# Kernel tuning notes

Measured on AMD Instinct MI355X. Metric: run time of the kernel, lower is better.

The kernel has to match this reference:

```python
import jax, jax.numpy as jnp
import numpy as np

HIDDEN = 1024
NH = 16
NKV = 8
HD = 128
ROPE_BASE = 1e6
EPS = 1e-6


def _rms_norm(x, w):
    # x: [..., HD], norm in fp32 like the torch module
    xf = x.astype(jnp.float32)
    var = jnp.mean(xf * xf, axis=-1, keepdims=True)
    return w * (xf * jax.lax.rsqrt(var + EPS)).astype(x.dtype)


def _rotate_half(x):
    h = x.shape[-1] // 2
    return jnp.concatenate([-x[..., h:], x[..., :h]], axis=-1)


def _rope_cos_sin(position_ids, dtype):
    inv_freq = 1.0 / (ROPE_BASE ** (jnp.arange(0, HD, 2, dtype=jnp.float32) / HD))
    freqs = position_ids.astype(jnp.float32)[:, None] * inv_freq[None, :]  # [S, HD/2]
    emb = jnp.concatenate([freqs, freqs], axis=-1)  # [S, HD]
    return jnp.cos(emb).astype(dtype), jnp.sin(emb).astype(dtype)


def setup_inputs() -> dict:
    key = jax.random.key(0)
    ks = jax.random.split(key, 7)
    B, S = 2, 2048
    scale = lambda fan_in: 1.0 / np.sqrt(fan_in)
    return {
        "hidden_states": jax.random.normal(ks[0], (B, S, HIDDEN), jnp.float32),
        "position_ids": jnp.arange(S, dtype=jnp.int32),
        "Wq": jax.random.normal(ks[1], (HIDDEN, NH * HD), jnp.float32) * scale(HIDDEN),
        "Wk": jax.random.normal(ks[2], (HIDDEN, NKV * HD), jnp.float32) * scale(HIDDEN),
        "Wv": jax.random.normal(ks[3], (HIDDEN, NKV * HD), jnp.float32) * scale(HIDDEN),
        "Wo": jax.random.normal(ks[4], (NH * HD, HIDDEN), jnp.float32) * scale(NH * HD),
        "q_norm_w": jnp.ones((HD,), jnp.float32),
        "k_norm_w": jnp.ones((HD,), jnp.float32),
    }


def reference(hidden_states, position_ids, Wq, Wk, Wv, Wo, q_norm_w, k_norm_w):
    B, S, _ = hidden_states.shape
    G = NH // NKV  # GQA group size

    q = (hidden_states @ Wq).reshape(B, S, NH, HD)
    k = (hidden_states @ Wk).reshape(B, S, NKV, HD)
    v = (hidden_states @ Wv).reshape(B, S, NKV, HD)

    q = _rms_norm(q, q_norm_w).transpose(0, 2, 1, 3)  # [B, NH, S, HD]
    k = _rms_norm(k, k_norm_w).transpose(0, 2, 1, 3)  # [B, NKV, S, HD]
    v = v.transpose(0, 2, 1, 3)                        # [B, NKV, S, HD]

    cos, sin = _rope_cos_sin(position_ids, q.dtype)    # [S, HD] each
    q = q * cos + _rotate_half(q) * sin
    k = k * cos + _rotate_half(k) * sin

    # GQA: broadcast KV heads across groups instead of repeat_interleave copies
    qg = q.reshape(B, NKV, G, S, HD)
    scores = jnp.einsum('bkgsd,bknd->bkgsn', qg, k) / jnp.sqrt(jnp.float32(HD))
    causal = jnp.tril(jnp.ones((S, S), dtype=bool))
    scores = jnp.where(causal, scores, -jnp.inf)
    attn = jax.nn.softmax(scores, axis=-1)
    out = jnp.einsum('bkgsn,bknd->bkgsd', attn, v)  # [B, NKV, G, S, HD]
    out = out.reshape(B, NH, S, HD).transpose(0, 2, 1, 3).reshape(B, S, NH * HD)
    return out @ Wo
```

## Files before the change

### kernel.cpp

```cpp
#include <hip/hip_runtime.h>
#include <cstdint>
#include <cstddef>

#define HIDDEN 1024
#define NH 16
#define NKV 8
#define HD 128
#define SEQ 2048
#define BATCH 2
#define NTOK (BATCH*SEQ)

typedef __bf16 bf16x8 __attribute__((ext_vector_type(8)));
typedef float f32x4 __attribute__((ext_vector_type(4)));

__device__ __forceinline__ unsigned short f2bf(float f) {
  unsigned int u = __float_as_uint(f);
  u += 0x7FFFu + ((u >> 16) & 1u);
  return (unsigned short)(u >> 16);
}
__device__ __forceinline__ float bf2f(unsigned short h) {
  return __uint_as_float(((unsigned int)h) << 16);
}

#if __has_builtin(__builtin_amdgcn_exp2f)
#define EXP2(x) __builtin_amdgcn_exp2f(x)
#else
#define EXP2(x) exp2f(x)
#endif

__device__ __forceinline__ void glds16(const unsigned short* g, unsigned short* l) {
  __builtin_amdgcn_global_load_lds(
      (const __attribute__((address_space(1))) unsigned int*)g,
      (__attribute__((address_space(3))) unsigned int*)l, 16, 0, 0);
}

#define WAIT_VM8()   __builtin_amdgcn_s_waitcnt(0x0F78)
#define WAIT_VM6()   __builtin_amdgcn_s_waitcnt(0x0F76)
#define WAIT_VM4()   __builtin_amdgcn_s_waitcnt(0x0F74)
#define WAIT_VM0()   __builtin_amdgcn_s_waitcnt(0x0F70)
#define WAIT_LGKM0() __builtin_amdgcn_s_waitcnt(0xC07F)
#define BARRIER()    __builtin_amdgcn_s_barrier()

__device__ __forceinline__ float dpp_addx1(float x) {
  int v = __builtin_amdgcn_update_dpp(0, __float_as_int(x), 0xB1, 0xF, 0xF, true);
  return x + __int_as_float(v);
}

__global__ __launch_bounds__(256) void tcvt_all_kernel(
    const float* __restrict__ Wq, const float* __restrict__ Wk,
    const float* __restrict__ Wv, const float* __restrict__ Wo,
    const float* __restrict__ hs,
    unsigned short* __restrict__ wqkvt, unsigned short* __restrict__ wot,
    unsigned short* __restrict__ hsb) {
  const int i = blockIdx.x;
  const int tx = threadIdx.x, ty = threadIdx.y;
  if (i >= 6144) {
    const int t = ty*32 + tx;
    const size_t base = (size_t)(i - 6144) * 1024;
#pragma unroll
    for (int j = 0; j < 4; ++j) {
      const size_t idx = base + j*256 + t;
      float4 v = ((const float4*)hs)[idx];
      ushort4 o;
      o.x = f2bf(v.x); o.y = f2bf(v.y); o.z = f2bf(v.z); o.w = f2bf(v.w);
      ((ushort4*)hsb)[idx] = o;
    }
    return;
  }
  __shared__ float tl[32][33];
  const float* src; unsigned short* dst; int R, C, r0, c0;
  if (i < 2048)      { int l = i;        src = Wq; dst = wqkvt;                      R = 1024; C = 2048; r0 = (l & 31)*32; c0 = (l >> 5)*32; }
  else if (i < 3072) { int l = i - 2048; src = Wk; dst = wqkvt + (size_t)2048*1024;  R = 1024; C = 1024; r0 = (l & 31)*32; c0 = (l >> 5)*32; }
  else if (i < 4096) { int l = i - 3072; src = Wv; dst = wqkvt + (size_t)3072*1024;  R = 1024; C = 1024; r0 = (l & 31)*32; c0 = (l >> 5)*32; }
  else               { int l = i - 4096; src = Wo; dst = wot;                        R = 2048; C = 1024; r0 = (l & 63)*32; c0 = (l >> 6)*32; }
#pragma unroll
  for (int k = 0; k < 4; ++k)
    tl[ty + 8*k][tx] = src[(size_t)(r0 + ty + 8*k)*C + c0 + tx];
  __syncthreads();
#pragma unroll
  for (int k = 0; k < 4; ++k)
    dst[(size_t)(c0 + ty + 8*k)*R + r0 + tx] = f2bf(tl[tx][ty + 8*k]);
}

__global__ __launch_bounds__(256) void gemm_qkv_fused_kernel(
    const unsigned short* __restrict__ A,
    const unsigned short* __restrict__ Bt,
    const float* __restrict__ qw, const float* __restrict__ kw,
    const int* __restrict__ pos_ids,
    unsigned short* __restrict__ q_l,
    unsigned short* __restrict__ k_l,
    unsigned short* __restrict__ vt8) {
  constexpr int BM = 128, BK = 64, K = 1024, NIT = K/BK;
  __shared__ __align__(16) char smem[70144];
  unsigned short* As0 = (unsigned short*)smem;
  unsigned short* Bs0 = (unsigned short*)(smem + 32768);
  float* ftile = (float*)smem;
  float* rinv  = (float*)(smem + 69632);

  const int t = threadIdx.x, lane = t & 63, w = t >> 6;
  const int l15 = lane & 15, l4 = lane >> 4;
  const int wr = (w >> 1)*64, wc = (w & 1)*64;
  const int m0 = blockIdx.x * BM, n0 = blockIdx.y * 128;
  const unsigned short* Ab = A + (size_t)m0*K;
  const unsigned short* Bb = Bt + (size_t)n0*K;

  const f32x4 vzero = {0.f, 0.f, 0.f, 0.f};
  f32x4 acc[4][4];
#pragma unroll
  for (int i = 0; i < 4; ++i)
#pragma unroll
    for (int j = 0; j < 4; ++j) acc[i][j] = vzero;

#pragma unroll
  for (int i = 0; i < 4; ++i) {
    const int c = (w*4 + i)*64 + lane;
    glds16(Ab + (size_t)(c >> 3)*K + (c & 7)*8, As0 + (size_t)(w*4 + i)*512);
  }
#pragma unroll
  for (int i = 0; i < 4; ++i) {
    const int c = (w*4 + i)*64 + lane;
    glds16(Bb + (size_t)(c >> 3)*K + (c & 7)*8, Bs0 + (size_t)(w*4 + i)*512);
  }

  for (int kb = 0; kb < NIT; ++kb) {
    const int cur = kb & 1;
    WAIT_LGKM0(); BARRIER();
    if (kb + 1 < NIT) {
      const int kn = (kb + 1) * BK;
      const int nb = (cur^1)*8192;
#pragma unroll
      for (int i = 0; i < 4; ++i) {
        const int c = (w*4 + i)*64 + lane;
        glds16(Ab + (size_t)(c >> 3)*K + kn + (c & 7)*8, As0 + nb + (size_t)(w*4 + i)*512);
      }
#pragma unroll
      for (int i = 0; i < 4; ++i) {
        const int c = (w*4 + i)*64 + lane;
        glds16(Bb + (size_t)(c >> 3)*K + kn + (c & 7)*8, Bs0 + nb + (size_t)(w*4 + i)*512);
      }
      WAIT_VM8();
    } else {
      WAIT_VM0();
    }
    BARRIER();

    const unsigned short* Ac = As0 + cur*8192;
    const unsigned short* Bc = Bs0 + cur*8192;
#pragma unroll
    for (int kk = 0; kk < 2; ++kk) {
      const int kc = kk*4 + l4;
      bf16x8 af[4], bfr[4];
#pragma unroll
      for (int i = 0; i < 4; ++i) {
        int m = wr + i*16 + l15;
        af[i] = *(const bf16x8*)(Ac + ((size_t)m*8 + kc)*8);
      }
#pragma unroll
      for (int j = 0; j < 4; ++j) {
        int n = wc + j*16 + l15;
        bfr[j] = *(const bf16x8*)(Bc + ((size_t)n*8 + kc)*8);
      }
#pragma unroll
      for (int i = 0; i < 4; ++i)
#pragma unroll
        for (int j = 0; j < 4; ++j)
          acc[i][j] = __builtin_amdgcn_mfma_f32_16x16x32_bf16(af[i], bfr[j], acc[i][j], 0, 0, 0);
    }
  }

  WAIT_LGKM0(); BARRIER();
#pragma unroll
  for (int i = 0; i < 4; ++i)
#pragma unroll
    for (int j = 0; j < 4; ++j)
#pragma unroll
      for (int r = 0; r < 4; ++r) {
        const int row = wr + i*16 + l4*4 + r;
        const int col = wc + j*16 + l15;
        ftile[row*136 + col] = acc[i][j][r];
      }
  WAIT_LGKM0(); BARRIER();

  const int ny = n0 >> 7;
  const int S0 = m0 & (SEQ-1);
  const int bb = m0 >> 11;

  if (ny < 24) {
    const bool isQ = ny < 16;
    {
      const int row = t >> 1, h2 = t & 1;
      const float* fr = ftile + row*136 + h2*64;
      float ssq = 0.f;
#pragma unroll
      for (int c = 0; c < 16; ++c) {
        float4 v = *(const float4*)(fr + 4*c);
        ssq += v.x*v.x + v.y*v.y + v.z*v.z + v.w*v.w;
      }
      ssq = dpp_addx1(ssq);
      if (h2 == 0) rinv[row] = rsqrtf(ssq*(1.0f/128.0f) + 1e-6f);
    }
    WAIT_LGKM0(); BARRIER();
    const float* wgt = isQ ? qw : kw;
    const int d = t & 127, rh = t >> 7;
    const float wd = wgt[d];
    const float w2 = wgt[d ^ 64];
    const float sgn = (d < 64) ? -1.f : 1.f;
    const float sOut = isQ ? 0.12751744f : 1.f;
    const float invf = exp2f(-(float)(d & 63) * 0.31143075889569023f);
    const int pos0 = pos_ids[S0 + rh*64];
    float cs, sn, dc, dsn;
    __sincosf((float)pos0 * invf, &sn, &cs);
    __sincosf(invf, &dsn, &dc);
    const int head = isQ ? ny : (ny - 16);
    unsigned short* dstb = isQ ? (q_l + ((size_t)(bb*NH + head)*SEQ + S0)*HD)
                               : (k_l + ((size_t)(bb*NKV + head)*SEQ + S0)*HD);
#pragma unroll 4
    for (int k = 0; k < 64; ++k) {
      const int row = rh*64 + k;
      const float r  = rinv[row];
      const float x1 = ftile[row*136 + d];
      const float x2 = ftile[row*136 + (d ^ 64)];
      const float y1 = x1*r*wd, y2 = x2*r*w2;
      const float o  = (y1*cs + sgn*(y2*sn)) * sOut;
      dstb[(size_t)row*HD + d] = f2bf(o);
      const float c2 = cs*dc - sn*dsn;
      sn = sn*dc + cs*dsn; cs = c2;
    }
  } else {
    const int vh = ny - 24;
    unsigned short* vb = vt8 + (size_t)(bb*NKV + vh)*HD*SEQ;
    const int d = t & 127, sbh = t >> 7;
#pragma unroll
    for (int sb = 0; sb < 8; ++sb) {
      const int sl = sbh*8 + sb;
      const int blk = sl >> 3, s = sl & 7;
      const int base_r = blk*64 + ((s>>2)<<5) + (((s>>1)&1)<<3) + ((s&1)<<2);
      union { unsigned short u[8]; uint4 q; } pk;
#pragma unroll
      for (int s8 = 0; s8 < 8; ++s8) {
        const int row = base_r + ((s8>>2)<<4) + (((s8>>1)&1)<<1) + (s8&1);
        pk.u[s8] = f2bf(ftile[row*136 + d]);
      }
      *(uint4*)(vb + ((size_t)((S0 >> 3) + sl)*128 + d)*8) = pk.q;
    }
  }
}

__global__ __launch_bounds__(256) void gemm_out_kernel(
    const unsigned short* __restrict__ A,
    const unsigned short* __restrict__ Bt,
    float* __restrict__ Cout, int M, int N, int K) {
  constexpr int BK = 64;
  __shared__ unsigned short As[2][128*BK];
  __shared__ unsigned short Bs[2][128*BK];
  const int t = threadIdx.x, lane = t & 63, w = t >> 6;
  const int l15 = lane & 15, l4 = lane >> 4;
  const int wr = (w >> 1)*64, wc = (w & 1)*64;
  const int m0 = blockIdx.y * 128, n0 = blockIdx.x * 128;
  const unsigned short* Ab = A + (size_t)m0*K;
  const unsigned short* Bb = Bt + (size_t)n0*K;

  const f32x4 vzero = {0.f, 0.f, 0.f, 0.f};
  f32x4 acc[4][4];
#pragma unroll
  for (int i = 0; i < 4; ++i)
#pragma unroll
    for (int j = 0; j < 4; ++j) acc[i][j] = vzero;

  const int NIT = K / BK;
#pragma unroll
  for (int i = 0; i < 4; ++i) {
    const int c = (w*4 + i)*64 + lane;
    glds16(Ab + (size_t)(c >> 3)*K + (c & 7)*8, &As[0][(size_t)(w*4 + i)*512]);
  }
#pragma unroll
  for (int i = 0; i < 4; ++i) {
    const int c = (w*4 + i)*64 + lane;
    glds16(Bb + (size_t)(c >> 3)*K + (c & 7)*8, &Bs[0][(size_t)(w*4 + i)*512]);
  }

  for (int kb = 0; kb < NIT; ++kb) {
    const int cur = kb & 1;
    WAIT_LGKM0(); BARRIER();
    if (kb + 1 < NIT) {
      const int kn = (kb + 1) * BK;
#pragma unroll
      for (int i = 0; i < 4; ++i) {
        const int c = (w*4 + i)*64 + lane;
        glds16(Ab + (size_t)(c >> 3)*K + kn + (c & 7)*8, &As[cur^1][(size_t)(w*4 + i)*512]);
      }
#pragma unroll
      for (int i = 0; i < 4; ++i) {
        const int c = (w*4 + i)*64 + lane;
        glds16(Bb + (size_t)(c >> 3)*K + kn + (c & 7)*8, &Bs[cur^1][(size_t)(w*4 + i)*512]);
      }
      WAIT_VM8();
    } else {
      WAIT_VM0();
    }
    BARRIER();

#pragma unroll
    for (int kk = 0; kk < 2; ++kk) {
      const int kc = kk*4 + l4;
      bf16x8 af[4], bfr[4];
#pragma unroll
      for (int i = 0; i < 4; ++i) {
        int m = wr + i*16 + l15;
        af[i] = *(const bf16x8*)(&As[cur][((size_t)m*8 + kc)*8]);
      }
#pragma unroll
      for (int j = 0; j < 4; ++j) {
        int n = wc + j*16 + l15;
        bfr[j] = *(const bf16x8*)(&Bs[cur][((size_t)n*8 + kc)*8]);
      }
#pragma unroll
      for (int i = 0; i < 4; ++i)
#pragma unroll
        for (int j = 0; j < 4; ++j)
          acc[i][j] = __builtin_amdgcn_mfma_f32_16x16x32_bf16(af[i], bfr[j], acc[i][j], 0, 0, 0);
    }
  }
#pragma unroll
  for (int i = 0; i < 4; ++i)
#pragma unroll
    for (int j = 0; j < 4; ++j)
#pragma unroll
      for (int r = 0; r < 4; ++r) {
        int row = m0 + wr + i*16 + l4*4 + r;
        int col = n0 + wc + j*16 + l15;
        Cout[(size_t)row*N + col] = acc[i][j][r];
      }
}

__global__ __launch_bounds__(256, 2) void attn_kernel(
    const unsigned short* __restrict__ q_l,
    const unsigned short* __restrict__ k_l,
    const unsigned short* __restrict__ vt8,
    unsigned short* __restrict__ o_part,
    float* __restrict__ l_part) {
  __shared__ __align__(16) char smem[65536];
  unsigned short* Ks0  = (unsigned short*)smem;
  unsigned short* Vts0 = (unsigned short*)(smem + 32768);

  const int t = threadIdx.x;
  const int lane = t & 63;
  const int w = t >> 6;
  const int l15 = lane & 15, l4 = lane >> 4;
  const int hb = blockIdx.x;
  const int h = hb & 15, b = hb >> 4;
  const int y = blockIdx.y;
  const int qt = 15 - (y >> 1);
  const int half = y & 1;
  const int kvh = h >> 1;
  const int q0 = qt * 128;
  const int kt0 = half ? (qt + 1) : 0;
  const int kt1 = half ? (2*qt + 2) : (qt + 1);

  const unsigned short* Kg = k_l + ((size_t)(b*NKV + kvh)*SEQ)*HD;
  const unsigned short* Vg = vt8 + (size_t)(b*NKV + kvh)*HD*SEQ;
  const unsigned short* Qbase = q_l + ((size_t)(b*NH + h)*SEQ)*HD;

  const f32x4 vzero = {0.f,0.f,0.f,0.f};

  bf16x8 qf[2][4];
#pragma unroll
  for (int i = 0; i < 2; ++i) {
    const int row = q0 + w*32 + i*16 + l15;
    const unsigned short* Qp = Qbase + (size_t)row*HD;
#pragma unroll
    for (int kk = 0; kk < 4; ++kk)
      qf[i][kk] = *(const bf16x8*)(Qp + kk*32 + l4*8);
  }

  f32x4 oacc[2][8];
#pragma unroll
  for (int i = 0; i < 2; ++i)
#pragma unroll
    for (int jd = 0; jd < 8; ++jd) oacc[i][jd] = vzero;
  float lrun[2] = {0.f, 0.f};

  {
    const int k00 = kt0 * 64;
#pragma unroll
    for (int i = 0; i < 4; ++i) {
      const int kc = w*4 + i;
      const int m = lane ^ (kc & 7);
      glds16(Kg + (size_t)(k00 + m)*HD + kc*8, Ks0 + (size_t)kc*64*8);
    }
#pragma unroll
    for (int i = 0; i < 4; ++i) {
      const int id = w*4 + i;
      const int skc = id >> 1, hh = id & 1;
      const int d = (hh*64 + lane) ^ skc;
      glds16(Vg + ((size_t)((k00 >> 3) + skc)*128 + d)*8, Vts0 + (size_t)(skc*128 + hh*64)*8);
    }
  }

#pragma unroll 1
  for (int kt = kt0; kt < kt1; ++kt) {
    const int cur = (kt - kt0) & 1;
    const int k0 = kt * 64;
    WAIT_LGKM0(); BARRIER();
    if (kt + 1 < kt1) {
      const int kn = k0 + 64;
      unsigned short* Ksn  = Ks0  + (cur^1)*8192;
      unsigned short* Vtsn = Vts0 + (cur^1)*8192;
#pragma unroll
      for (int i = 0; i < 4; ++i) {
        const int kc = w*4 + i;
        const int m = lane ^ (kc & 7);
        glds16(Kg + (size_t)(kn + m)*HD + kc*8, Ksn + (size_t)kc*64*8);
      }
#pragma unroll
      for (int i = 0; i < 4; ++i) {
        const int id = w*4 + i;
        const int skc = id >> 1, hh = id & 1;
        const int d = (hh*64 + lane) ^ skc;
        glds16(Vg + ((size_t)((kn >> 3) + skc)*128 + d)*8, Vtsn + (size_t)(skc*128 + hh*64)*8);
      }
      WAIT_VM8();
    } else {
      WAIT_VM0();
    }
    BARRIER();

    const unsigned short* KsC  = Ks0  + cur*8192;
    const unsigned short* VtsC = Vts0 + cur*8192;

    f32x4 sacc[4][2];
#pragma unroll
    for (int j = 0; j < 4; ++j)
#pragma unroll
      for (int i = 0; i < 2; ++i) sacc[j][i] = vzero;
    __builtin_amdgcn_s_setprio(1);
#pragma unroll
    for (int kk = 0; kk < 4; ++kk) {
      const int kc = kk*4 + l4;
      bf16x8 kb[4];
#pragma unroll
      for (int j = 0; j < 4; ++j) {
        int n = j*16 + l15;
        kb[j] = *(const bf16x8*)(KsC + ((size_t)kc*64 + (n ^ (kc & 7)))*8);
      }
#pragma unroll
      for (int j = 0; j < 4; ++j)
#pragma unroll
        for (int i = 0; i < 2; ++i)
          sacc[j][i] = __builtin_amdgcn_mfma_f32_16x16x32_bf16(kb[j], qf[i][kk], sacc[j][i], 0,0,0);
    }
    __builtin_amdgcn_s_setprio(0);

    const bool diag = (kt >= 2*qt);
#pragma unroll
    for (int j = 0; j < 4; ++j)
#pragma unroll
      for (int i = 0; i < 2; ++i)
#pragma unroll
        for (int r = 0; r < 4; ++r) {
          float sv = sacc[j][i][r];
          if (diag) {
            const int kvg = k0 + j*16 + l4*4 + r;
            const int qg  = q0 + w*32 + i*16 + l15;
            sv = (kvg > qg) ? -INFINITY : sv;
          }
          float pv = EXP2(sv);
          sacc[j][i][r] = pv;
          lrun[i] += pv;
        }

#pragma unroll
    for (int kk = 0; kk < 2; ++kk) {
      union { unsigned int u[4]; bf16x8 v; } pb[2];
#pragma unroll
      for (int i = 0; i < 2; ++i) {
        const f32x4 t0 = sacc[kk*2][i], t1 = sacc[kk*2+1][i];
        pb[i].u[0] = (__float_as_uint(t0[0]) >> 16) | (__float_as_uint(t0[1]) & 0xFFFF0000u);
        pb[i].u[1] = (__float_as_uint(t0[2]) >> 16) | (__float_as_uint(t0[3]) & 0xFFFF0000u);
        pb[i].u[2] = (__float_as_uint(t1[0]) >> 16) | (__float_as_uint(t1[1]) & 0xFFFF0000u);
        pb[i].u[3] = (__float_as_uint(t1[2]) >> 16) | (__float_as_uint(t1[3]) & 0xFFFF0000u);
      }
      const int s = kk*4 + l4;
      __builtin_amdgcn_s_setprio(1);
#pragma unroll
      for (int td = 0; td < 8; ++td) {
        const int dd = td*16 + l15;
        bf16x8 va = *(const bf16x8*)(VtsC + ((size_t)s*128 + (dd ^ s))*8);
#pragma unroll
        for (int i = 0; i < 2; ++i)
          oacc[i][td] = __builtin_amdgcn_mfma_f32_16x16x32_bf16(va, pb[i].v, oacc[i][td], 0,0,0);
      }
      __builtin_amdgcn_s_setprio(0);
    }
  }

  unsigned short* ob = o_part + ((size_t)half*BATCH*NH*SEQ + (size_t)(b*NH + h)*SEQ)*HD;
  float* lb = l_part + (size_t)half*BATCH*NH*SEQ + (size_t)(b*NH + h)*SEQ;
#pragma unroll
  for (int i = 0; i < 2; ++i) {
    float lsum = lrun[i];
    lsum += __shfl_xor(lsum, 16, 64);
    lsum += __shfl_xor(lsum, 32, 64);
    const float inv = (lsum > 0.f) ? 1.0f / lsum : 0.f;
    const int row = q0 + w*32 + i*16 + l15;
    if (l4 == 0) lb[row] = lsum;
#pragma unroll
    for (int td = 0; td < 8; ++td) {
      union { unsigned int u[2]; uint2 q; } pk;
      const float v0 = oacc[i][td][0]*inv, v1 = oacc[i][td][1]*inv;
      const float v2 = oacc[i][td][2]*inv, v3 = oacc[i][td][3]*inv;
      pk.u[0] = (unsigned int)f2bf(v0) | ((unsigned int)f2bf(v1) << 16);
      pk.u[1] = (unsigned int)f2bf(v2) | ((unsigned int)f2bf(v3) << 16);
      *(uint2*)(ob + (size_t)row*HD + td*16 + l4*4) = pk.q;
    }
  }
}

__global__ __launch_bounds__(256) void combine_kernel(
    const unsigned short* __restrict__ o_part,
    const float* __restrict__ l_part,
    unsigned short* __restrict__ attn_o) {
  const int tid = blockIdx.x * 256 + threadIdx.x;
  const int d8 = tid & 15;
  const int row = tid >> 4;
  const int s = row & (SEQ-1);
  const int bh = row >> 11;
  const int h = bh & 15, b = bh >> 4;
  const float la = l_part[row];
  const float lbv = l_part[BATCH*NH*SEQ + row];
  const float inv = 1.f / (la + lbv);
  const float wa = la * inv, wb = lbv * inv;
  const unsigned short* pa = o_part + (size_t)row*HD + d8*8;
  const unsigned short* pb = pa + (size_t)BATCH*NH*SEQ*HD;
  uint4 ua = *(const uint4*)pa;
  uint4 ub = *(const uint4*)pb;
  const unsigned short* ea = (const unsigned short*)&ua;
  const unsigned short* eb = (const unsigned short*)&ub;
  union { unsigned short u[8]; uint4 q; } o;
#pragma unroll
  for (int k = 0; k < 8; ++k)
    o.u[k] = f2bf(bf2f(ea[k])*wa + bf2f(eb[k])*wb);
  *(uint4*)(attn_o + ((size_t)(b*SEQ + s)*(NH*HD)) + h*HD + d8*8) = o.q;
}

extern "C" void kernel_launch(void* const* d_in, const int* in_sizes, int n_in,
                              void* d_out, int out_size, void* d_ws, size_t ws_size,
                              hipStream_t stream) {
  const float* hs = (const float*)d_in[0];
  const int* pos  = (const int*)d_in[1];
  const float* Wq = (const float*)d_in[2];
  const float* Wk = (const float*)d_in[3];
  const float* Wv = (const float*)d_in[4];
  const float* Wo = (const float*)d_in[5];
  const float* qw = (const float*)d_in[6];
  const float* kw = (const float*)d_in[7];
  float* out = (float*)d_out;
  char* ws = (char*)d_ws;

  unsigned short* attn_o = (unsigned short*)(ws + 0);
  unsigned short* wot    = (unsigned short*)(ws + ((size_t)16 << 20));
  unsigned short* q_l    = (unsigned short*)(ws + ((size_t)20 << 20));
  unsigned short* k_l    = (unsigned short*)(ws + ((size_t)36 << 20));
  unsigned short* vt8    = (unsigned short*)(ws + ((size_t)44 << 20));
  unsigned short* o_part = (unsigned short*)(ws + ((size_t)52 << 20));
  unsigned short* hsb    = (unsigned short*)(ws + ((size_t)52 << 20));
  unsigned short* wqkvt  = (unsigned short*)(ws + ((size_t)60 << 20));
  float*          l_part = (float*)(ws + ((size_t)84 << 20));

  tcvt_all_kernel<<<dim3(7168), dim3(32, 8), 0, stream>>>(Wq, Wk, Wv, Wo, hs, wqkvt, wot, hsb);
  gemm_qkv_fused_kernel<<<dim3(32, 32), dim3(256), 0, stream>>>(hsb, wqkvt, qw, kw, pos, q_l, k_l, vt8);
  attn_kernel<<<dim3(32, 32), dim3(256), 0, stream>>>(q_l, k_l, vt8, o_part, l_part);
  combine_kernel<<<dim3(4096), dim3(256), 0, stream>>>(o_part, l_part, attn_o);
  gemm_out_kernel<<<dim3(8, 32), dim3(256), 0, stream>>>(attn_o, wot, out, 4096, 1024, 2048);
}
```

Before: 258.2 us.

## Share KV tiles across both GQA heads in 512-thread attention blocks

The attention kernel now launches 512-thread blocks, one per (batch, KV head), and the two query heads of a GQA group each get four waves. Every K/V tile loaded into LDS is therefore reused by both heads, halving KV global traffic per query. The query tile shrinks from 128 to 64 rows, with each wave handling 16 rows. The KV range is split evenly in two halves per query tile, which changes the grid to 16x64. The risks are a smaller per-wave MMA tile with fewer registers per wave, more blocks to schedule, and the new 4-blocks-per-CU launch bound against a 64 KB LDS footprint.

New measurement: 256.4 us. No clear change (-0.7%).

```diff
diff --git a/kernel.cpp b/kernel.cpp
--- a/kernel.cpp
+++ b/kernel.cpp
@@ -35,7 +35,6 @@
 }
 
 #define WAIT_VM8()   __builtin_amdgcn_s_waitcnt(0x0F78)
-#define WAIT_VM6()   __builtin_amdgcn_s_waitcnt(0x0F76)
 #define WAIT_VM4()   __builtin_amdgcn_s_waitcnt(0x0F74)
 #define WAIT_VM0()   __builtin_amdgcn_s_waitcnt(0x0F70)
 #define WAIT_LGKM0() __builtin_amdgcn_s_waitcnt(0xC07F)
@@ -333,7 +332,7 @@
       }
 }
 
-__global__ __launch_bounds__(256, 2) void attn_kernel(
+__global__ __launch_bounds__(512, 4) void attn_kernel(
     const unsigned short* __restrict__ q_l,
     const unsigned short* __restrict__ k_l,
     const unsigned short* __restrict__ vt8,
@@ -347,15 +346,18 @@
   const int lane = t & 63;
   const int w = t >> 6;
   const int l15 = lane & 15, l4 = lane >> 4;
-  const int hb = blockIdx.x;
-  const int h = hb & 15, b = hb >> 4;
+  const int p = blockIdx.x;
+  const int kvh = p & 7, b = p >> 3;
+  const int h = kvh*2 + (w >> 2);
+  const int wq = w & 3;
   const int y = blockIdx.y;
-  const int qt = 15 - (y >> 1);
+  const int qt = 31 - (y >> 1);
   const int half = y & 1;
-  const int kvh = h >> 1;
-  const int q0 = qt * 128;
-  const int kt0 = half ? (qt + 1) : 0;
-  const int kt1 = half ? (2*qt + 2) : (qt + 1);
+  const int q0 = qt * 64;
+  const int T  = qt + 1;
+  const int h0 = (T + 1) >> 1;
+  const int kt0 = half ? h0 : 0;
+  const int kt1 = half ? T : h0;
 
   const unsigned short* Kg = k_l + ((size_t)(b*NKV + kvh)*SEQ)*HD;
   const unsigned short* Vg = vt8 + (size_t)(b*NKV + kvh)*HD*SEQ;
@@ -363,152 +365,141 @@
 
   const f32x4 vzero = {0.f,0.f,0.f,0.f};
 
-  bf16x8 qf[2][4];
-#pragma unroll
-  for (int i = 0; i < 2; ++i) {
-    const int row = q0 + w*32 + i*16 + l15;
+  bf16x8 qf[4];
+  {
+    const int row = q0 + wq*16 + l15;
     const unsigned short* Qp = Qbase + (size_t)row*HD;
 #pragma unroll
     for (int kk = 0; kk < 4; ++kk)
-      qf[i][kk] = *(const bf16x8*)(Qp + kk*32 + l4*8);
-  }
-
-  f32x4 oacc[2][8];
-#pragma unroll
-  for (int i = 0; i < 2; ++i)
-#pragma unroll
-    for (int jd = 0; jd < 8; ++jd) oacc[i][jd] = vzero;
-  float lrun[2] = {0.f, 0.f};
-
-  {
-    const int k00 = kt0 * 64;
-#pragma unroll
-    for (int i = 0; i < 4; ++i) {
-      const int kc = w*4 + i;
-      const int m = lane ^ (kc & 7);
-      glds16(Kg + (size_t)(k00 + m)*HD + kc*8, Ks0 + (size_t)kc*64*8);
-    }
-#pragma unroll
-    for (int i = 0; i < 4; ++i) {
-      const int id = w*4 + i;
-      const int skc = id >> 1, hh = id & 1;
-      const int d = (hh*64 + lane) ^ skc;
-      glds16(Vg + ((size_t)((k00 >> 3) + skc)*128 + d)*8, Vts0 + (size_t)(skc*128 + hh*64)*8);
-    }
-  }
-
-#pragma unroll 1
-  for (int kt = kt0; kt < kt1; ++kt) {
-    const int cur = (kt - kt0) & 1;
-    const int k0 = kt * 64;
-    WAIT_LGKM0(); BARRIER();
-    if (kt + 1 < kt1) {
-      const int kn = k0 + 64;
-      unsigned short* Ksn  = Ks0  + (cur^1)*8192;
-      unsigned short* Vtsn = Vts0 + (cur^1)*8192;
-#pragma unroll
-      for (int i = 0; i < 4; ++i) {
-        const int kc = w*4 + i;
+      qf[kk] = *(const bf16x8*)(Qp + kk*32 + l4*8);
+  }
+
+  f32x4 oacc[8];
+#pragma unroll
+  for (int jd = 0; jd < 8; ++jd) oacc[jd] = vzero;
+  float lrun = 0.f;
+
+  if (kt0 < kt1) {
+    {
+      const int k00 = kt0 * 64;
+#pragma unroll
+      for (int i = 0; i < 2; ++i) {
+        const int kc = w*2 + i;
         const int m = lane ^ (kc & 7);
-        glds16(Kg + (size_t)(kn + m)*HD + kc*8, Ksn + (size_t)kc*64*8);
-      }
-#pragma unroll
-      for (int i = 0; i < 4; ++i) {
-        const int id = w*4 + i;
+        glds16(Kg + (size_t)(k00 + m)*HD + kc*8, Ks0 + (size_t)kc*64*8);
+      }
+#pragma unroll
+      for (int i = 0; i < 2; ++i) {
+        const int id = w*2 + i;
         const int skc = id >> 1, hh = id & 1;
         const int d = (hh*64 + lane) ^ skc;
-        glds16(Vg + ((size_t)((kn >> 3) + skc)*128 + d)*8, Vtsn + (size_t)(skc*128 + hh*64)*8);
-      }
-      WAIT_VM8();
-    } else {
-      WAIT_VM0();
-    }
-    BARRIER();
-
-    const unsigned short* KsC  = Ks0  + cur*8192;
-    const unsigned short* VtsC = Vts0 + cur*8192;
-
-    f32x4 sacc[4][2];
-#pragma unroll
-    for (int j = 0; j < 4; ++j)
-#pragma unroll
-      for (int i = 0; i < 2; ++i) sacc[j][i] = vzero;
-    __builtin_amdgcn_s_setprio(1);
-#pragma unroll
-    for (int kk = 0; kk < 4; ++kk) {
-      const int kc = kk*4 + l4;
-      bf16x8 kb[4];
-#pragma unroll
-      for (int j = 0; j < 4; ++j) {
-        int n = j*16 + l15;
-        kb[j] = *(const bf16x8*)(KsC + ((size_t)kc*64 + (n ^ (kc & 7)))*8);
-      }
+        glds16(Vg + ((size_t)((k00 >> 3) + skc)*128 + d)*8, Vts0 + (size_t)(skc*128 + hh*64)*8);
+      }
+    }
+
+#pragma unroll 1
+    for (int kt = kt0; kt < kt1; ++kt) {
+      const int cur = (kt - kt0) & 1;
+      const int k0 = kt * 64;
+      WAIT_LGKM0(); BARRIER();
+      if (kt + 1 < kt1) {
+        const int kn = k0 + 64;
+        unsigned short* Ksn  = Ks0  + (cur^1)*8192;
+        unsigned short* Vtsn = Vts0 + (cur^1)*8192;
+#pragma unroll
+        for (int i = 0; i < 2; ++i) {
+          const int kc = w*2 + i;
+          const int m = lane ^ (kc & 7);
+          glds16(Kg + (size_t)(kn + m)*HD + kc*8, Ksn + (size_t)kc*64*8);
+        }
+#pragma unroll
+        for (int i = 0; i < 2; ++i) {
+          const int id = w*2 + i;
+          const int skc = id >> 1, hh = id & 1;
+          const int d = (hh*64 + lane) ^ skc;
+          glds16(Vg + ((size_t)((kn >> 3) + skc)*128 + d)*8, Vtsn + (size_t)(skc*128 + hh*64)*8);
+        }
+        WAIT_VM4();
+      } else {
+        WAIT_VM0();
+      }
+      BARRIER();
+
+      const unsigned short* KsC  = Ks0  + cur*8192;
+      const unsigned short* VtsC = Vts0 + cur*8192;
+
+      f32x4 sacc[4];
+#pragma unroll
+      for (int j = 0; j < 4; ++j) sacc[j] = vzero;
+      __builtin_amdgcn_s_setprio(1);
+#pragma unroll
+      for (int kk = 0; kk < 4; ++kk) {
+        const int kc = kk*4 + l4;
+        bf16x8 kb[4];
+#pragma unroll
+        for (int j = 0; j < 4; ++j) {
+          int n = j*16 + l15;
+          kb[j] = *(const bf16x8*)(KsC + ((size_t)kc*64 + (n ^ (kc & 7)))*8);
+        }
+#pragma unroll
+        for (int j = 0; j < 4; ++j)
+          sacc[j] = __builtin_amdgcn_mfma_f32_16x16x32_bf16(kb[j], qf[kk], sacc[j], 0,0,0);
+      }
+      __builtin_amdgcn_s_setprio(0);
+
+      const bool diag = (kt == qt);
 #pragma unroll
       for (int j = 0; j < 4; ++j)
 #pragma unroll
-        for (int i = 0; i < 2; ++i)
-          sacc[j][i] = __builtin_amdgcn_mfma_f32_16x16x32_bf16(kb[j], qf[i][kk], sacc[j][i], 0,0,0);
-    }
-    __builtin_amdgcn_s_setprio(0);
-
-    const bool diag = (kt >= 2*qt);
-#pragma unroll
-    for (int j = 0; j < 4; ++j)
-#pragma unroll
-      for (int i = 0; i < 2; ++i)
-#pragma unroll
         for (int r = 0; r < 4; ++r) {
-          float sv = sacc[j][i][r];
+          float sv = sacc[j][r];
           if (diag) {
             const int kvg = k0 + j*16 + l4*4 + r;
-            const int qg  = q0 + w*32 + i*16 + l15;
+            const int qg  = q0 + wq*16 + l15;
             sv = (kvg > qg) ? -INFINITY : sv;
           }
           float pv = EXP2(sv);
-          sacc[j][i][r] = pv;
-          lrun[i] += pv;
+          sacc[j][r] = pv;
+          lrun += pv;
         }
 
 #pragma unroll
-    for (int kk = 0; kk < 2; ++kk) {
-      union { unsigned int u[4]; bf16x8 v; } pb[2];
-#pragma unroll
-      for (int i = 0; i < 2; ++i) {
-        const f32x4 t0 = sacc[kk*2][i], t1 = sacc[kk*2+1][i];
-        pb[i].u[0] = (__float_as_uint(t0[0]) >> 16) | (__float_as_uint(t0[1]) & 0xFFFF0000u);
-        pb[i].u[1] = (__float_as_uint(t0[2]) >> 16) | (__float_as_uint(t0[3]) & 0xFFFF0000u);
-        pb[i].u[2] = (__float_as_uint(t1[0]) >> 16) | (__float_as_uint(t1[1]) & 0xFFFF0000u);
-        pb[i].u[3] = (__float_as_uint(t1[2]) >> 16) | (__float_as_uint(t1[3]) & 0xFFFF0000u);
-      }
-      const int s = kk*4 + l4;
-      __builtin_amdgcn_s_setprio(1);
-#pragma unroll
-      for (int td = 0; td < 8; ++td) {
-        const int dd = td*16 + l15;
-        bf16x8 va = *(const bf16x8*)(VtsC + ((size_t)s*128 + (dd ^ s))*8);
-#pragma unroll
-        for (int i = 0; i < 2; ++i)
-          oacc[i][td] = __builtin_amdgcn_mfma_f32_16x16x32_bf16(va, pb[i].v, oacc[i][td], 0,0,0);
-      }
-      __builtin_amdgcn_s_setprio(0);
+      for (int kk = 0; kk < 2; ++kk) {
+        union { unsigned int u[4]; bf16x8 v; } pb;
+        {
+          const f32x4 t0 = sacc[kk*2], t1 = sacc[kk*2+1];
+          pb.u[0] = (__float_as_uint(t0[0]) >> 16) | (__float_as_uint(t0[1]) & 0xFFFF0000u);
+          pb.u[1] = (__float_as_uint(t0[2]) >> 16) | (__float_as_uint(t0[3]) & 0xFFFF0000u);
+          pb.u[2] = (__float_as_uint(t1[0]) >> 16) | (__float_as_uint(t1[1]) & 0xFFFF0000u);
+          pb.u[3] = (__float_as_uint(t1[2]) >> 16) | (__float_as_uint(t1[3]) & 0xFFFF0000u);
+        }
+        const int s = kk*4 + l4;
+        __builtin_amdgcn_s_setprio(1);
+#pragma unroll
+        for (int td = 0; td < 8; ++td) {
+          const int dd = td*16 + l15;
+          bf16x8 va = *(const bf16x8*)(VtsC + ((size_t)s*128 + (dd ^ s))*8);
+          oacc[td] = __builtin_amdgcn_mfma_f32_16x16x32_bf16(va, pb.v, oacc[td], 0,0,0);
+        }
+        __builtin_amdgcn_s_setprio(0);
+      }
     }
   }
 
   unsigned short* ob = o_part + ((size_t)half*BATCH*NH*SEQ + (size_t)(b*NH + h)*SEQ)*HD;
   float* lb = l_part + (size_t)half*BATCH*NH*SEQ + (size_t)(b*NH + h)*SEQ;
-#pragma unroll
-  for (int i = 0; i < 2; ++i) {
-    float lsum = lrun[i];
+  {
+    float lsum = lrun;
     lsum += __shfl_xor(lsum, 16, 64);
     lsum += __shfl_xor(lsum, 32, 64);
     const float inv = (lsum > 0.f) ? 1.0f / lsum : 0.f;
-    const int row = q0 + w*32 + i*16 + l15;
+    const int row = q0 + wq*16 + l15;
     if (l4 == 0) lb[row] = lsum;
 #pragma unroll
     for (int td = 0; td < 8; ++td) {
       union { unsigned int u[2]; uint2 q; } pk;
-      const float v0 = oacc[i][td][0]*inv, v1 = oacc[i][td][1]*inv;
-      const float v2 = oacc[i][td][2]*inv, v3 = oacc[i][td][3]*inv;
+      const float v0 = oacc[td][0]*inv, v1 = oacc[td][1]*inv;
+      const float v2 = oacc[td][2]*inv, v3 = oacc[td][3]*inv;
       pk.u[0] = (unsigned int)f2bf(v0) | ((unsigned int)f2bf(v1) << 16);
       pk.u[1] = (unsigned int)f2bf(v2) | ((unsigned int)f2bf(v3) << 16);
       *(uint2*)(ob + (size_t)row*HD + td*16 + l4*4) = pk.q;
@@ -569,7 +560,7 @@
 
   tcvt_all_kernel<<<dim3(7168), dim3(32, 8), 0, stream>>>(Wq, Wk, Wv, Wo, hs, wqkvt, wot, hsb);
   gemm_qkv_fused_kernel<<<dim3(32, 32), dim3(256), 0, stream>>>(hsb, wqkvt, qw, kw, pos, q_l, k_l, vt8);
-  attn_kernel<<<dim3(32, 32), dim3(256), 0, stream>>>(q_l, k_l, vt8, o_part, l_part);
+  attn_kernel<<<dim3(16, 64), dim3(512), 0, stream>>>(q_l, k_l, vt8, o_part, l_part);
   combine_kernel<<<dim3(4096), dim3(256), 0, stream>>>(o_part, l_part, attn_o);
   gemm_out_kernel<<<dim3(8, 32), dim3(256), 0, stream>>>(attn_o, wot, out, 4096, 1024, 2048);
 }
```
